# Optimization experiments

Measured on AMD Instinct MI355X. Metric: run time of the kernel, lower is better.

The kernel has to match this reference:

```python
import jax, jax.numpy as jnp
import numpy as np

MAX_ATOMS = 14  # hard-coded padded atom slots per residue in the original module


def setup_inputs() -> dict:
    key = jax.random.key(0)
    k1, k2, k3 = jax.random.split(key, 3)
    N_RES = 100000
    C = 128  # config.m; OutputLayer(3) emits m channels, fc1 = Linear(14*m, 1)
    feature = jax.random.normal(k1, (N_RES * MAX_ATOMS, C), dtype=jnp.float32)
    atom_num = jax.random.randint(k2, (N_RES,), 0, MAX_ATOMS, dtype=jnp.int32)
    label_binary = jax.random.randint(k3, (N_RES,), 0, 2, dtype=jnp.int32)
    return {"feature": feature, "atom_num": atom_num, "label_binary": label_binary}


def reference(feature, atom_num, label_binary):
    # Ragged gather-to-padded: atoms of residue r live at flat positions
    # [offset[r], offset[r]+atom_num[r]) in `feature`; copy into slot [r, :atom_num[r], :]
    # of a zero-padded [N_res, 14, C] tensor (the original nested Python loop).
    counts = atom_num.astype(jnp.int32)
    offsets = jnp.concatenate([jnp.zeros((1,), jnp.int32), jnp.cumsum(counts)[:-1]])  # [N_res]
    slots = jnp.arange(MAX_ATOMS, dtype=jnp.int32)                                    # [14]
    idx = offsets[:, None] + slots[None, :]                                           # [N_res, 14]
    mask = slots[None, :] < counts[:, None]                                           # [N_res, 14]
    idx = jnp.clip(idx, 0, feature.shape[0] - 1)
    padded = feature[idx] * mask[:, :, None].astype(feature.dtype)                    # [N_res, 14, C]
    aa_feature = padded.reshape(padded.shape[0], -1)                                  # [N_res, 14*C]
    return aa_feature, label_binary
```

## Files before the change

kernel.cpp:

```cpp
#include <hip/hip_runtime.h>


#define MAX_ATOMS 14
#define CCH 128
#define F4_PER_ROW 32
#define F4_PER_RES (MAX_ATOMS * F4_PER_ROW)
#define RPB 16

__global__ void k_block_sums(const int* __restrict__ atom_num, int n,
                             int* __restrict__ sums) {
    __shared__ int lds[256];
    int t = threadIdx.x;
    int r = blockIdx.x * 256 + t;
    lds[t] = (r < n) ? atom_num[r] : 0;
    __syncthreads();
    for (int d = 128; d > 0; d >>= 1) {
        if (t < d) lds[t] += lds[t + d];
        __syncthreads();
    }
    if (t == 0) sums[blockIdx.x] = lds[0];
}

__global__ void k_scan_sums(int* __restrict__ sums, int nb) {
    __shared__ int lds[512];
    int t = threadIdx.x;
    int v = (t < nb) ? sums[t] : 0;
    lds[t] = v;
    __syncthreads();
    for (int d = 1; d < 512; d <<= 1) {
        int add = (t >= d) ? lds[t - d] : 0;
        __syncthreads();
        lds[t] += add;
        __syncthreads();
    }
    if (t < nb) sums[t] = lds[t] - v;
}

__global__ void k_offsets(const int* __restrict__ atom_num, int n,
                          const int* __restrict__ scanned,
                          int* __restrict__ offsets) {
    __shared__ int lds[256];
    int t = threadIdx.x;
    int r = blockIdx.x * 256 + t;
    int v = (r < n) ? atom_num[r] : 0;
    lds[t] = v;
    __syncthreads();
    for (int d = 1; d < 256; d <<= 1) {
        int add = (t >= d) ? lds[t - d] : 0;
        __syncthreads();
        lds[t] += add;
        __syncthreads();
    }
    if (r < n) offsets[r] = scanned[blockIdx.x] + lds[t] - v;
}

__global__ void k_gather(const float4* __restrict__ feat,
                         const int* __restrict__ atom_num,
                         const int* __restrict__ offsets,
                         const int* __restrict__ label,
                         float4* __restrict__ out,
                         float* __restrict__ out_label,
                         int n) {
    __shared__ int off_s[RPB];
    __shared__ int cnt_s[RPB];
    int t = threadIdx.x;
    int rbase = blockIdx.x * RPB;
    if (t < RPB) {
        int r = rbase + t;
        if (r < n) {
            off_s[t] = offsets[r];
            cnt_s[t] = atom_num[r];
            out_label[r] = (float)label[r];
        } else {
            off_s[t] = 0;
            cnt_s[t] = 0;
        }
    }
    __syncthreads();

    #pragma unroll 4
    for (int e = t; e < RPB * F4_PER_RES; e += 256) {
        int rl   = e / F4_PER_RES;
        int rem  = e - rl * F4_PER_RES;
        int slot = rem >> 5;
        int r = rbase + rl;
        if (r < n) {
            float4 val = make_float4(0.f, 0.f, 0.f, 0.f);
            if (slot < cnt_s[rl]) {
                val = feat[(size_t)(off_s[rl] + slot) * F4_PER_ROW + (rem & 31)];
            }
            out[(size_t)r * F4_PER_RES + rem] = val;
        }
    }
}

extern "C" void kernel_launch(void* const* d_in, const int* in_sizes, int n_in,
                              void* d_out, int out_size, void* d_ws, size_t ws_size,
                              hipStream_t stream) {
    const float* feature = (const float*)d_in[0];
    const int* atom_num  = (const int*)d_in[1];
    const int* label     = (const int*)d_in[2];
    const int n = in_sizes[1];

    float* out = (float*)d_out;
    float* out_label = out + (size_t)n * MAX_ATOMS * CCH;

    int* ws_offsets = (int*)d_ws;
    int* ws_sums    = ws_offsets + n;

    int nb = (n + 255) / 256;
    k_block_sums<<<nb, 256, 0, stream>>>(atom_num, n, ws_sums);
    k_scan_sums<<<1, 512, 0, stream>>>(ws_sums, nb);
    k_offsets<<<nb, 256, 0, stream>>>(atom_num, n, ws_sums, ws_offsets);

    int gb = (n + RPB - 1) / RPB;
    k_gather<<<gb, 256, 0, stream>>>((const float4*)feature, atom_num,
                                     ws_offsets, label,
                                     (float4*)out, out_label, n);
}
```

Before: 226.8 us.

## Fuse offset scan into gather and use nontemporal loads/stores

Drops the separate offsets kernel: the first kernel now writes per-block local exclusive offsets, and the gather adds the scanned block base when it loads each residue's offset. This removes one kernel launch and one pass over atom_num. The gather loop gets a fixed trip count with a fast path for full blocks, and uses nontemporal loads and stores so the streaming traffic does not pollute cache. The output is about 717 MB, so the gather dominates, and the nontemporal hints may help or hurt bandwidth.

```diff
diff --git a/kernel.cpp b/kernel.cpp
--- a/kernel.cpp
+++ b/kernel.cpp
@@ -6,19 +6,27 @@
 #define F4_PER_ROW 32
 #define F4_PER_RES (MAX_ATOMS * F4_PER_ROW)
 #define RPB 16
+#define ITERS ((RPB * F4_PER_RES) / 256)
 
-__global__ void k_block_sums(const int* __restrict__ atom_num, int n,
+typedef float f32x4 __attribute__((ext_vector_type(4)));
+
+__global__ void k_local_scan(const int* __restrict__ atom_num, int n,
+                             int* __restrict__ local_off,
                              int* __restrict__ sums) {
     __shared__ int lds[256];
     int t = threadIdx.x;
     int r = blockIdx.x * 256 + t;
-    lds[t] = (r < n) ? atom_num[r] : 0;
+    int v = (r < n) ? atom_num[r] : 0;
+    lds[t] = v;
     __syncthreads();
-    for (int d = 128; d > 0; d >>= 1) {
-        if (t < d) lds[t] += lds[t + d];
+    for (int d = 1; d < 256; d <<= 1) {
+        int add = (t >= d) ? lds[t - d] : 0;
+        __syncthreads();
+        lds[t] += add;
         __syncthreads();
     }
-    if (t == 0) sums[blockIdx.x] = lds[0];
+    if (r < n) local_off[r] = lds[t] - v;
+    if (t == 255) sums[blockIdx.x] = lds[255];
 }
 
 __global__ void k_scan_sums(int* __restrict__ sums, int nb) {
@@ -36,31 +44,15 @@
     if (t < nb) sums[t] = lds[t] - v;
 }
 
-__global__ void k_offsets(const int* __restrict__ atom_num, int n,
-                          const int* __restrict__ scanned,
-                          int* __restrict__ offsets) {
-    __shared__ int lds[256];
-    int t = threadIdx.x;
-    int r = blockIdx.x * 256 + t;
-    int v = (r < n) ? atom_num[r] : 0;
-    lds[t] = v;
-    __syncthreads();
-    for (int d = 1; d < 256; d <<= 1) {
-        int add = (t >= d) ? lds[t - d] : 0;
-        __syncthreads();
-        lds[t] += add;
-        __syncthreads();
-    }
-    if (r < n) offsets[r] = scanned[blockIdx.x] + lds[t] - v;
-}
-
-__global__ void k_gather(const float4* __restrict__ feat,
-                         const int* __restrict__ atom_num,
-                         const int* __restrict__ offsets,
-                         const int* __restrict__ label,
-                         float4* __restrict__ out,
-                         float* __restrict__ out_label,
-                         int n) {
+__global__ __launch_bounds__(256) void k_gather(
+        const f32x4* __restrict__ feat,
+        const int* __restrict__ atom_num,
+        const int* __restrict__ local_off,
+        const int* __restrict__ block_base,
+        const int* __restrict__ label,
+        f32x4* __restrict__ out,
+        float* __restrict__ out_label,
+        int n) {
     __shared__ int off_s[RPB];
     __shared__ int cnt_s[RPB];
     int t = threadIdx.x;
@@ -68,7 +60,7 @@
     if (t < RPB) {
         int r = rbase + t;
         if (r < n) {
-            off_s[t] = offsets[r];
+            off_s[t] = block_base[rbase >> 8] + local_off[r];
             cnt_s[t] = atom_num[r];
             out_label[r] = (float)label[r];
         } else {
@@ -78,18 +70,36 @@
     }
     __syncthreads();
 
-    #pragma unroll 4
-    for (int e = t; e < RPB * F4_PER_RES; e += 256) {
-        int rl   = e / F4_PER_RES;
-        int rem  = e - rl * F4_PER_RES;
-        int slot = rem >> 5;
-        int r = rbase + rl;
-        if (r < n) {
-            float4 val = make_float4(0.f, 0.f, 0.f, 0.f);
+    if (rbase + RPB <= n) {
+        #pragma unroll 7
+        for (int i = 0; i < ITERS; ++i) {
+            int e    = t + i * 256;
+            int rl   = e / F4_PER_RES;
+            int rem  = e - rl * F4_PER_RES;
+            int slot = rem >> 5;
+            f32x4 val = (f32x4)0.f;
             if (slot < cnt_s[rl]) {
-                val = feat[(size_t)(off_s[rl] + slot) * F4_PER_ROW + (rem & 31)];
+                val = __builtin_nontemporal_load(
+                    &feat[(size_t)(off_s[rl] + slot) * F4_PER_ROW + (rem & 31)]);
             }
-            out[(size_t)r * F4_PER_RES + rem] = val;
+            __builtin_nontemporal_store(val,
+                &out[(size_t)rbase * F4_PER_RES + e]);
+        }
+    } else {
+        for (int i = 0; i < ITERS; ++i) {
+            int e    = t + i * 256;
+            int rl   = e / F4_PER_RES;
+            int rem  = e - rl * F4_PER_RES;
+            int slot = rem >> 5;
+            if (rbase + rl < n) {
+                f32x4 val = (f32x4)0.f;
+                if (slot < cnt_s[rl]) {
+                    val = __builtin_nontemporal_load(
+                        &feat[(size_t)(off_s[rl] + slot) * F4_PER_ROW + (rem & 31)]);
+                }
+                __builtin_nontemporal_store(val,
+                    &out[(size_t)rbase * F4_PER_RES + e]);
+            }
         }
     }
 }
@@ -105,16 +115,15 @@
     float* out = (float*)d_out;
     float* out_label = out + (size_t)n * MAX_ATOMS * CCH;
 
-    int* ws_offsets = (int*)d_ws;
-    int* ws_sums    = ws_offsets + n;
+    int* ws_local = (int*)d_ws;
+    int* ws_sums  = ws_local + n;
 
     int nb = (n + 255) / 256;
-    k_block_sums<<<nb, 256, 0, stream>>>(atom_num, n, ws_sums);
+    k_local_scan<<<nb, 256, 0, stream>>>(atom_num, n, ws_local, ws_sums);
     k_scan_sums<<<1, 512, 0, stream>>>(ws_sums, nb);
-    k_offsets<<<nb, 256, 0, stream>>>(atom_num, n, ws_sums, ws_offsets);
 
     int gb = (n + RPB - 1) / RPB;
-    k_gather<<<gb, 256, 0, stream>>>((const float4*)feature, atom_num,
-                                     ws_offsets, label,
-                                     (float4*)out, out_label, n);
+    k_gather<<<gb, 256, 0, stream>>>((const f32x4*)feature, atom_num,
+                                     ws_local, ws_sums, label,
+                                     (f32x4*)out, out_label, n);
 }
```

Measured after the change: 219.6 us. 3.2% less time.
